# Kernel optimization log

Hardware: AMD Instinct MI355X
Metric: run time of the kernel (lower is better)

## Reference

```python
import jax, jax.numpy as jnp
import numpy as np

EPS = 1e-6
N_HEADS = 16


def _stable_softmax(x):
    # max subtracted with stop_gradient (torch .detach()), clamp to [-50, 50], eps in denom
    x_max = jax.lax.stop_gradient(jnp.max(x, axis=-1, keepdims=True))
    exp_x = jnp.exp(jnp.clip(x - x_max, -50.0, 50.0))
    return exp_x / (jnp.sum(exp_x, axis=-1, keepdims=True) + EPS)


def setup_inputs() -> dict:
    key = jax.random.key(0)
    k1, k2, k3 = jax.random.split(key, 3)
    B, S, D = 2, 2048, 1024
    x = jax.random.normal(k1, (B, S, D), dtype=jnp.float32)
    Wqkv = jax.random.normal(k2, (3 * D, D), dtype=jnp.float32) * 0.02
    Wout = jax.random.normal(k3, (D, D), dtype=jnp.float32) * (0.02 / np.sqrt(2))
    return {"x": x, "Wqkv": Wqkv, "Wout": Wout}


def reference(x, Wqkv, Wout):
    B, S, D = x.shape
    H = N_HEADS
    Dh = D // H
    scale = 1.0 / np.sqrt(Dh)
    # qkv projection (torch Linear: x @ W.T), split into q,k,v -> (B,H,S,Dh)
    qkv = (x @ Wqkv.T).reshape(B, S, 3, H, Dh)
    qkv = jnp.transpose(qkv, (2, 0, 3, 1, 4))
    q, k, v = qkv[0], qkv[1], qkv[2]
    # chunked attention is mathematically identical to full attention here
    scores = jnp.einsum('bhqd,bhkd->bhqk', q, k) * scale
    attn = _stable_softmax(scores)
    out = jnp.einsum('bhqk,bhkd->bhqd', attn, v)  # (B,H,S,Dh)
    out = jnp.transpose(out, (0, 2, 1, 3)).reshape(B, S, D)
    return out @ Wout.T
```

## Files before the change

### kernel.cpp

```cpp
#include <hip/hip_runtime.h>
#include <hip/hip_bf16.h>
#include <stdint.h>

#define S_LEN   2048
#define D_MODEL 1024
#define NH      16
#define DH      64
#define BATCH   2
#define TOKENS  (BATCH * S_LEN)

typedef __bf16 bf16;
typedef __bf16 bf16x8 __attribute__((ext_vector_type(8)));
typedef __bf16 b16x4  __attribute__((ext_vector_type(4)));
typedef float  f32x4  __attribute__((ext_vector_type(4)));
typedef float  f32x16 __attribute__((ext_vector_type(16)));
typedef unsigned int uint32;

__device__ __forceinline__ void async_lds16(const void* g, void* l) {
  __builtin_amdgcn_global_load_lds((__attribute__((address_space(1))) void*)g,
                                   (__attribute__((address_space(3))) void*)l,
                                   16, 0, 0);
}

__global__ __launch_bounds__(256) void convert_kernel(
    const float* __restrict__ src, bf16* __restrict__ dst, int n8) {
  const int i = blockIdx.x * 256 + threadIdx.x;
  if (i >= n8) return;
  const f32x4 a = *(const f32x4*)(src + (size_t)i * 8);
  const f32x4 b = *(const f32x4*)(src + (size_t)i * 8 + 4);
  bf16x8 o;
#pragma unroll
  for (int j = 0; j < 4; j++) { o[j] = (bf16)a[j]; o[j + 4] = (bf16)b[j]; }
  *(bf16x8*)(dst + (size_t)i * 8) = o;
}

#define BM 128
#define BN 128
#define BK 32

#define GEMM_CORE(APTR, BPTR, KDIM)                                              \
  __shared__ __align__(16) bf16 As[BM * BK];                                     \
  __shared__ __align__(16) bf16 Bs[BN * BK];                                     \
  const int tid  = threadIdx.x;                                                  \
  const int wave = tid >> 6, lane = tid & 63;                                    \
  const int quad = lane >> 4, l16 = lane & 15;                                   \
  const int id   = blockIdx.y * gridDim.x + blockIdx.x;                          \
  const int xcd  = id & 7, lin = id >> 3;                                        \
  const int ccols = gridDim.x >> 1, crows = gridDim.y >> 2;                      \
  const int m0 = ((xcd >> 1) * crows + lin / ccols) * BM;                        \
  const int n0 = ((xcd & 1) * ccols + lin % ccols) * BN;                         \
  const int wm = (wave >> 1) * 64, wn = (wave & 1) * 64;                         \
  f32x4 acc[4][4] = {};                                                          \
  const int c0 = tid, c1 = tid + 256;                                            \
  for (int k0 = 0; k0 < (KDIM); k0 += BK) {                                      \
    async_lds16((APTR) + (size_t)(m0 + (c0 >> 2)) * (KDIM) + k0 + (c0 & 3) * 8,  \
                As + c0 * 8);                                                    \
    async_lds16((APTR) + (size_t)(m0 + (c1 >> 2)) * (KDIM) + k0 + (c1 & 3) * 8,  \
                As + c1 * 8);                                                    \
    async_lds16((BPTR) + (size_t)(n0 + (c0 >> 2)) * (KDIM) + k0 + (c0 & 3) * 8,  \
                Bs + c0 * 8);                                                    \
    async_lds16((BPTR) + (size_t)(n0 + (c1 >> 2)) * (KDIM) + k0 + (c1 & 3) * 8,  \
                Bs + c1 * 8);                                                    \
    __syncthreads();                                                             \
    bf16x8 af[4], bfr[4];                                                        \
    _Pragma("unroll") for (int i = 0; i < 4; i++)                                \
        af[i] = *(const bf16x8*)(As + (wm + i * 16 + l16) * BK + quad * 8);      \
    _Pragma("unroll") for (int j = 0; j < 4; j++)                                \
        bfr[j] = *(const bf16x8*)(Bs + (wn + j * 16 + l16) * BK + quad * 8);     \
    _Pragma("unroll") for (int i = 0; i < 4; i++)                                \
      _Pragma("unroll") for (int j = 0; j < 4; j++)                              \
        acc[i][j] = __builtin_amdgcn_mfma_f32_16x16x32_bf16(af[i], bfr[j],       \
                                                            acc[i][j], 0, 0, 0); \
    __syncthreads();                                                             \
  }

__global__ __launch_bounds__(256) void gemm_qkv_kernel(
    const bf16* __restrict__ X, const bf16* __restrict__ W,
    bf16* __restrict__ Qo, bf16* __restrict__ Ko, bf16* __restrict__ VTo) {
  GEMM_CORE(X, W, D_MODEL)
  const int t = n0 >> 10;
#pragma unroll
  for (int i = 0; i < 4; i++) {
    const int rowb = m0 + wm + i * 16 + quad * 4;
    const int b = rowb >> 11, s0 = rowb & 2047;
#pragma unroll
    for (int j = 0; j < 4; j++) {
      const int col = n0 + wn + j * 16 + l16;
      const int h = (col >> 6) & 15, d = col & 63;
      if (t == 2) {
        b16x4 v4;
#pragma unroll
        for (int r = 0; r < 4; r++) v4[r] = (bf16)acc[i][j][r];
        *(b16x4*)(VTo + ((size_t)(b * NH + h) * DH + d) * S_LEN + s0) = v4;
      } else {
#pragma unroll
        for (int r = 0; r < 4; r++) {
          const float v = acc[i][j][r];
          if (t == 0)
            Qo[((size_t)(b * NH + h) * S_LEN + s0 + r) * DH + d] = (bf16)(v * 0.125f);
          else
            Ko[((size_t)(b * NH + h) * S_LEN + s0 + r) * DH + d] = (bf16)v;
        }
      }
    }
  }
}

__global__ __launch_bounds__(256) void gemm_out_kernel(
    const bf16* __restrict__ A, const bf16* __restrict__ W,
    float* __restrict__ Out) {
  GEMM_CORE(A, W, D_MODEL)
#pragma unroll
  for (int i = 0; i < 4; i++) {
    const int rowb = m0 + wm + i * 16 + quad * 4;
#pragma unroll
    for (int j = 0; j < 4; j++) {
      const int col = n0 + wn + j * 16 + l16;
#pragma unroll
      for (int r = 0; r < 4; r++)
        Out[(size_t)(rowb + r) * D_MODEL + col] = acc[i][j][r];
    }
  }
}

__global__ __launch_bounds__(512, 2) void attn_kernel(
    const bf16* __restrict__ Q, const bf16* __restrict__ K,
    const bf16* __restrict__ VT, bf16* __restrict__ AO) {
  __shared__ __align__(16) bf16 smem[2][2][2 * 64 * 64];

  const int tid  = threadIdx.x;
  const int lane = tid & 63;
  const int wave = tid >> 6;
  const int g    = wave >> 2;
  const int qw   = wave & 3;
  const int l31  = lane & 31;
  const int hi   = lane >> 5;
  const int sw   = l31 & 7;

  const int bid = (blockIdx.x & 7) * 32 + (blockIdx.x >> 3);
  const int qb  = bid & 7;
  const int bh  = bid >> 3;

  const bf16* qp = Q  + ((size_t)bh * S_LEN + qb * 256 + qw * 64 + l31) * DH;
  const bf16* kp = K  + (size_t)bh * S_LEN * DH;
  const bf16* vp = VT + (size_t)bh * DH * S_LEN;

  bf16x8 qf0[4], qf1[4];
#pragma unroll
  for (int dk = 0; dk < 4; dk++) {
    qf0[dk] = *(const bf16x8*)(qp + dk * 16 + hi * 8);
    qf1[dk] = *(const bf16x8*)(qp + 32 * DH + dk * 16 + hi * 8);
  }

  const int gtid = tid & 255;
  const int cid0 = gtid, cid1 = gtid + 256;
  const int r0 = cid0 >> 3, c0 = (cid0 & 7) ^ (r0 & 7);
  const int r1 = cid1 >> 3, c1 = (cid1 & 7) ^ (r1 & 7);
  const bf16* ka0 = kp + (size_t)(g * 64 + r0) * DH + c0 * 8;
  const bf16* ka1 = kp + (size_t)(g * 64 + r1) * DH + c1 * 8;
  const bf16* va0 = vp + (size_t)r0 * S_LEN + g * 64 + c0 * 8;
  const bf16* va1 = vp + (size_t)r1 * S_LEN + g * 64 + c1 * 8;
  const int ld0 = cid0 * 8, ld1 = cid1 * 8;

  f32x16 oT0[2] = {}, oT1[2] = {};
  float lsum0 = 0.f, lsum1 = 0.f;

  bf16* sg = &smem[g][0][0];

#define STAGE(B)                                                                 \
  {                                                                              \
    bf16* s = sg + (B) * (2 * 64 * 64);                                          \
    async_lds16(ka0, s + ld0);                                                   \
    async_lds16(ka1, s + ld1);                                                   \
    async_lds16(va0, s + 4096 + ld0);                                            \
    async_lds16(va1, s + 4096 + ld1);                                            \
    ka0 += 8192; ka1 += 8192; va0 += 128; va1 += 128;                            \
  }

  STAGE(0)

#pragma unroll 2
  for (int t = 0; t < 16; t++) {
    const int cur = t & 1;
    asm volatile("s_waitcnt vmcnt(0)" ::: "memory");
    __builtin_amdgcn_s_barrier();
    if (t < 15) {
      STAGE(cur ^ 1)
    }

    const bf16* sb = sg + cur * (2 * 64 * 64);

    bf16x8 vfr[8];
#pragma unroll
    for (int dt = 0; dt < 2; dt++)
#pragma unroll
      for (int ks = 0; ks < 4; ks++)
        vfr[dt * 4 + ks] = *(const bf16x8*)(sb + 4096 + (dt * 32 + l31) * 64 +
                                            (((ks * 2 + hi) ^ sw) * 8));

    f32x16 st0[2] = {}, st1[2] = {};
    __builtin_amdgcn_s_setprio(1);
#pragma unroll
    for (int kt = 0; kt < 2; kt++)
#pragma unroll
      for (int dk = 0; dk < 4; dk++) {
        const bf16x8 kf = *(const bf16x8*)(sb + (kt * 32 + l31) * 64 +
                                           (((dk * 2 + hi) ^ sw) * 8));
        st0[kt] = __builtin_amdgcn_mfma_f32_32x32x16_bf16(kf, qf0[dk], st0[kt], 0, 0, 0);
        st1[kt] = __builtin_amdgcn_mfma_f32_32x32x16_bf16(kf, qf1[dk], st1[kt], 0, 0, 0);
      }
    __builtin_amdgcn_s_setprio(0);

#pragma unroll
    for (int kt = 0; kt < 2; kt++)
#pragma unroll
      for (int hk = 0; hk < 2; hk++) {
        const int ks = kt * 2 + hk;
        float e0[8], e1[8];
#pragma unroll
        for (int r = 0; r < 8; r++) e0[r] = __expf(st0[kt][hk * 8 + r]);
#pragma unroll
        for (int r = 0; r < 8; r++) e1[r] = __expf(st1[kt][hk * 8 + r]);
        lsum0 += ((e0[0] + e0[1]) + (e0[2] + e0[3])) + ((e0[4] + e0[5]) + (e0[6] + e0[7]));
        lsum1 += ((e1[0] + e1[1]) + (e1[2] + e1[3])) + ((e1[4] + e1[5]) + (e1[6] + e1[7]));
        uint32 p00, p01, p02, p03, p10, p11, p12, p13;
        asm("v_cvt_pk_bf16_f32 %0, %1, %2" : "=v"(p00) : "v"(e0[0]), "v"(e0[1]));
        asm("v_cvt_pk_bf16_f32 %0, %1, %2" : "=v"(p01) : "v"(e0[2]), "v"(e0[3]));
        asm("v_cvt_pk_bf16_f32 %0, %1, %2" : "=v"(p02) : "v"(e0[4]), "v"(e0[5]));
        asm("v_cvt_pk_bf16_f32 %0, %1, %2" : "=v"(p03) : "v"(e0[6]), "v"(e0[7]));
        asm("v_cvt_pk_bf16_f32 %0, %1, %2" : "=v"(p10) : "v"(e1[0]), "v"(e1[1]));
        asm("v_cvt_pk_bf16_f32 %0, %1, %2" : "=v"(p11) : "v"(e1[2]), "v"(e1[3]));
        asm("v_cvt_pk_bf16_f32 %0, %1, %2" : "=v"(p12) : "v"(e1[4]), "v"(e1[5]));
        asm("v_cvt_pk_bf16_f32 %0, %1, %2" : "=v"(p13) : "v"(e1[6]), "v"(e1[7]));
        asm("v_permlane32_swap_b32 %0, %1" : "+v"(p00), "+v"(p02));
        asm("v_permlane32_swap_b32 %0, %1" : "+v"(p01), "+v"(p03));
        asm("v_permlane32_swap_b32 %0, %1" : "+v"(p10), "+v"(p12));
        asm("v_permlane32_swap_b32 %0, %1" : "+v"(p11), "+v"(p13));
        union { uint32 u[4]; bf16x8 v; } pf0, pf1;
        pf0.u[0] = p00; pf0.u[1] = p01; pf0.u[2] = p02; pf0.u[3] = p03;
        pf1.u[0] = p10; pf1.u[1] = p11; pf1.u[2] = p12; pf1.u[3] = p13;
        __builtin_amdgcn_s_setprio(1);
#pragma unroll
        for (int dt = 0; dt < 2; dt++) {
          oT0[dt] = __builtin_amdgcn_mfma_f32_32x32x16_bf16(vfr[dt * 4 + ks], pf0.v,
                                                            oT0[dt], 0, 0, 0);
          oT1[dt] = __builtin_amdgcn_mfma_f32_32x32x16_bf16(vfr[dt * 4 + ks], pf1.v,
                                                            oT1[dt], 0, 0, 0);
        }
        __builtin_amdgcn_s_setprio(0);
      }
  }
#undef STAGE

  __syncthreads();

  lsum0 += __shfl_xor(lsum0, 32);
  lsum1 += __shfl_xor(lsum1, 32);

  float* mO = (float*)&smem[0][0][0];
  float* mL = mO + 256 * 32;
  const int mrow = qw * 64 + lane;

  if (g == 1) {
#pragma unroll
    for (int j = 0; j < 8; j++) {
      const int dt = j >> 2, rb = (j & 3) * 4;
      f32x4 c = { oT0[dt][rb], oT0[dt][rb + 1], oT0[dt][rb + 2], oT0[dt][rb + 3] };
      *(f32x4*)((char*)mO + mrow * 128 + ((j ^ (lane & 7)) * 16)) = c;
    }
    mL[mrow] = lsum0;
  }
  __syncthreads();
  if (g == 0) {
#pragma unroll
    for (int j = 0; j < 8; j++) {
      const int dt = j >> 2, rb = (j & 3) * 4;
      const f32x4 c = *(const f32x4*)((char*)mO + mrow * 128 + ((j ^ (lane & 7)) * 16));
#pragma unroll
      for (int rr = 0; rr < 4; rr++) oT0[dt][rb + rr] += c[rr];
    }
    lsum0 += mL[mrow];
  }
  __syncthreads();
  if (g == 1) {
#pragma unroll
    for (int j = 0; j < 8; j++) {
      const int dt = j >> 2, rb = (j & 3) * 4;
      f32x4 c = { oT1[dt][rb], oT1[dt][rb + 1], oT1[dt][rb + 2], oT1[dt][rb + 3] };
      *(f32x4*)((char*)mO + mrow * 128 + ((j ^ (lane & 7)) * 16)) = c;
    }
    mL[mrow] = lsum1;
  }
  __syncthreads();
  if (g == 0) {
#pragma unroll
    for (int j = 0; j < 8; j++) {
      const int dt = j >> 2, rb = (j & 3) * 4;
      const f32x4 c = *(const f32x4*)((char*)mO + mrow * 128 + ((j ^ (lane & 7)) * 16));
#pragma unroll
      for (int rr = 0; rr < 4; rr++) oT1[dt][rb + rr] += c[rr];
    }
    lsum1 += mL[mrow];

    const float inv0 = 1.0f / (lsum0 + 1e-6f);
    const float inv1 = 1.0f / (lsum1 + 1e-6f);
    const int b = bh >> 4, h = bh & 15;
    const int srow = qb * 256 + qw * 64 + l31;
    const size_t base0 = (size_t)(b * S_LEN + srow) * D_MODEL + h * DH;
    const size_t base1 = base0 + (size_t)32 * D_MODEL;
#pragma unroll
    for (int dt = 0; dt < 2; dt++)
#pragma unroll
      for (int rg = 0; rg < 4; rg++) {
        b16x4 o4;
#pragma unroll
        for (int rr = 0; rr < 4; rr++) o4[rr] = (bf16)(oT0[dt][rg * 4 + rr] * inv0);
        *(b16x4*)(AO + base0 + dt * 32 + rg * 8 + hi * 4) = o4;
      }
#pragma unroll
    for (int dt = 0; dt < 2; dt++)
#pragma unroll
      for (int rg = 0; rg < 4; rg++) {
        b16x4 o4;
#pragma unroll
        for (int rr = 0; rr < 4; rr++) o4[rr] = (bf16)(oT1[dt][rg * 4 + rr] * inv1);
        *(b16x4*)(AO + base1 + dt * 32 + rg * 8 + hi * 4) = o4;
      }
  }
}

extern "C" void kernel_launch(void* const* d_in, const int* in_sizes, int n_in,
                              void* d_out, int out_size, void* d_ws, size_t ws_size,
                              hipStream_t stream) {
  const float* x    = (const float*)d_in[0];
  const float* wqkv = (const float*)d_in[1];
  const float* wout = (const float*)d_in[2];
  float* out = (float*)d_out;

  bf16* Q  = (bf16*)d_ws;
  bf16* K  = Q  + (size_t)TOKENS * D_MODEL;
  bf16* VT = K  + (size_t)TOKENS * D_MODEL;
  bf16* xb = VT + (size_t)TOKENS * D_MODEL;
  bf16* AO = xb;
  bf16* wqkvb = (bf16*)d_out;
  bf16* woutb = Q;

  convert_kernel<<<dim3(TOKENS * D_MODEL / (256 * 8)), dim3(256), 0, stream>>>(
      x, xb, TOKENS * D_MODEL / 8);
  convert_kernel<<<dim3(3 * D_MODEL * D_MODEL / (256 * 8)), dim3(256), 0, stream>>>(
      wqkv, wqkvb, 3 * D_MODEL * D_MODEL / 8);

  gemm_qkv_kernel<<<dim3(3 * D_MODEL / BN, TOKENS / BM), dim3(256), 0, stream>>>(
      xb, wqkvb, Q, K, VT);

  attn_kernel<<<dim3(BATCH * NH * (S_LEN / 256)), dim3(512), 0, stream>>>(Q, K, VT, AO);

  convert_kernel<<<dim3(D_MODEL * D_MODEL / (256 * 8)), dim3(256), 0, stream>>>(
      wout, woutb, D_MODEL * D_MODEL / 8);

  gemm_out_kernel<<<dim3(D_MODEL / BN, TOKENS / BM), dim3(256), 0, stream>>>(
      AO, woutb, out);
}
```

Measured before the change: 193.7 us.

## Merge input conversions, fuse Wout conversion into output GEMM, drop XCD tile swizzle

Combines the x and Wqkv fp32-to-bf16 conversions into a single launch. The separate Wout conversion kernel is removed: the output GEMM now loads fp32 Wout tiles directly, converts them in registers and writes bf16 into LDS. The XCD-aware block remapping in the GEMMs is replaced by plain blockIdx tiling. This saves two launches and a pass over Wout, but the output GEMM now does synchronous fp32 loads of twice the bytes (Wout is converted once per row tile), and the simpler mapping may reduce L2 locality.

```diff
diff --git a/kernel.cpp b/kernel.cpp
--- a/kernel.cpp
+++ b/kernel.cpp
@@ -22,16 +22,25 @@
                                    16, 0, 0);
 }
 
-__global__ __launch_bounds__(256) void convert_kernel(
-    const float* __restrict__ src, bf16* __restrict__ dst, int n8) {
-  const int i = blockIdx.x * 256 + threadIdx.x;
-  if (i >= n8) return;
-  const f32x4 a = *(const f32x4*)(src + (size_t)i * 8);
-  const f32x4 b = *(const f32x4*)(src + (size_t)i * 8 + 4);
+__global__ __launch_bounds__(256) void convert2_kernel(
+    const float* __restrict__ s0, bf16* __restrict__ d0, int n0,
+    const float* __restrict__ s1, bf16* __restrict__ d1, int n1) {
+  int i = blockIdx.x * 256 + threadIdx.x;
+  const float* s;
+  bf16* d;
+  if (i < n0) {
+    s = s0 + (size_t)i * 8; d = d0 + (size_t)i * 8;
+  } else {
+    i -= n0;
+    if (i >= n1) return;
+    s = s1 + (size_t)i * 8; d = d1 + (size_t)i * 8;
+  }
+  const f32x4 a = *(const f32x4*)s;
+  const f32x4 b = *(const f32x4*)(s + 4);
   bf16x8 o;
 #pragma unroll
   for (int j = 0; j < 4; j++) { o[j] = (bf16)a[j]; o[j + 4] = (bf16)b[j]; }
-  *(bf16x8*)(dst + (size_t)i * 8) = o;
+  *(bf16x8*)d = o;
 }
 
 #define BM 128
@@ -44,11 +53,8 @@
   const int tid  = threadIdx.x;                                                  \
   const int wave = tid >> 6, lane = tid & 63;                                    \
   const int quad = lane >> 4, l16 = lane & 15;                                   \
-  const int id   = blockIdx.y * gridDim.x + blockIdx.x;                          \
-  const int xcd  = id & 7, lin = id >> 3;                                        \
-  const int ccols = gridDim.x >> 1, crows = gridDim.y >> 2;                      \
-  const int m0 = ((xcd >> 1) * crows + lin / ccols) * BM;                        \
-  const int n0 = ((xcd & 1) * ccols + lin % ccols) * BN;                         \
+  const int m0 = blockIdx.y * BM;                                                \
+  const int n0 = blockIdx.x * BN;                                                \
   const int wm = (wave >> 1) * 64, wn = (wave & 1) * 64;                         \
   f32x4 acc[4][4] = {};                                                          \
   const int c0 = tid, c1 = tid + 256;                                            \
@@ -107,9 +113,53 @@
 }
 
 __global__ __launch_bounds__(256) void gemm_out_kernel(
-    const bf16* __restrict__ A, const bf16* __restrict__ W,
+    const bf16* __restrict__ A, const float* __restrict__ WF,
     float* __restrict__ Out) {
-  GEMM_CORE(A, W, D_MODEL)
+  __shared__ __align__(16) bf16 As[BM * BK];
+  __shared__ __align__(16) bf16 Bs[BN * BK];
+  const int tid  = threadIdx.x;
+  const int wave = tid >> 6, lane = tid & 63;
+  const int quad = lane >> 4, l16 = lane & 15;
+  const int m0 = blockIdx.y * BM;
+  const int n0 = blockIdx.x * BN;
+  const int wm = (wave >> 1) * 64, wn = (wave & 1) * 64;
+  f32x4 acc[4][4] = {};
+  const int c0 = tid, c1 = tid + 256;
+  for (int k0 = 0; k0 < D_MODEL; k0 += BK) {
+    async_lds16(A + (size_t)(m0 + (c0 >> 2)) * D_MODEL + k0 + (c0 & 3) * 8,
+                As + c0 * 8);
+    async_lds16(A + (size_t)(m0 + (c1 >> 2)) * D_MODEL + k0 + (c1 & 3) * 8,
+                As + c1 * 8);
+    {
+      const float* wp0 = WF + (size_t)(n0 + (c0 >> 2)) * D_MODEL + k0 + (c0 & 3) * 8;
+      const float* wp1 = WF + (size_t)(n0 + (c1 >> 2)) * D_MODEL + k0 + (c1 & 3) * 8;
+      const f32x4 a0 = *(const f32x4*)wp0, b0 = *(const f32x4*)(wp0 + 4);
+      const f32x4 a1 = *(const f32x4*)wp1, b1 = *(const f32x4*)(wp1 + 4);
+      bf16x8 v0, v1;
+#pragma unroll
+      for (int j = 0; j < 4; j++) {
+        v0[j] = (bf16)a0[j]; v0[j + 4] = (bf16)b0[j];
+        v1[j] = (bf16)a1[j]; v1[j + 4] = (bf16)b1[j];
+      }
+      *(bf16x8*)(Bs + c0 * 8) = v0;
+      *(bf16x8*)(Bs + c1 * 8) = v1;
+    }
+    __syncthreads();
+    bf16x8 af[4], bfr[4];
+#pragma unroll
+    for (int i = 0; i < 4; i++)
+      af[i] = *(const bf16x8*)(As + (wm + i * 16 + l16) * BK + quad * 8);
+#pragma unroll
+    for (int j = 0; j < 4; j++)
+      bfr[j] = *(const bf16x8*)(Bs + (wn + j * 16 + l16) * BK + quad * 8);
+#pragma unroll
+    for (int i = 0; i < 4; i++)
+#pragma unroll
+      for (int j = 0; j < 4; j++)
+        acc[i][j] = __builtin_amdgcn_mfma_f32_16x16x32_bf16(af[i], bfr[j],
+                                                            acc[i][j], 0, 0, 0);
+    __syncthreads();
+  }
 #pragma unroll
   for (int i = 0; i < 4; i++) {
     const int rowb = m0 + wm + i * 16 + quad * 4;
@@ -343,21 +393,17 @@
   bf16* xb = VT + (size_t)TOKENS * D_MODEL;
   bf16* AO = xb;
   bf16* wqkvb = (bf16*)d_out;
-  bf16* woutb = Q;
-
-  convert_kernel<<<dim3(TOKENS * D_MODEL / (256 * 8)), dim3(256), 0, stream>>>(
-      x, xb, TOKENS * D_MODEL / 8);
-  convert_kernel<<<dim3(3 * D_MODEL * D_MODEL / (256 * 8)), dim3(256), 0, stream>>>(
-      wqkv, wqkvb, 3 * D_MODEL * D_MODEL / 8);
+
+  const int nx = TOKENS * D_MODEL / 8;
+  const int nw = 3 * D_MODEL * D_MODEL / 8;
+  convert2_kernel<<<dim3((nx + nw) / 256), dim3(256), 0, stream>>>(
+      x, xb, nx, wqkv, wqkvb, nw);
 
   gemm_qkv_kernel<<<dim3(3 * D_MODEL / BN, TOKENS / BM), dim3(256), 0, stream>>>(
       xb, wqkvb, Q, K, VT);
 
   attn_kernel<<<dim3(BATCH * NH * (S_LEN / 256)), dim3(512), 0, stream>>>(Q, K, VT, AO);
 
-  convert_kernel<<<dim3(D_MODEL * D_MODEL / (256 * 8)), dim3(256), 0, stream>>>(
-      wout, woutb, D_MODEL * D_MODEL / 8);
-
   gemm_out_kernel<<<dim3(D_MODEL / BN, TOKENS / BM), dim3(256), 0, stream>>>(
-      AO, woutb, out);
-}
+      AO, wout, out);
+}
```

New measurement: 187.4 us. 3.2% less time.
